# Performance work log

Measured on AMD Instinct MI355X. Metric: run time of the kernel, lower is better.

Reference implementation:

```python
import jax, jax.numpy as jnp
import numpy as np

N_G, E_G, E_H, E_I = 100000, 1000000, 1500000, 2000000
IN_FEATS = 64


def setup_inputs() -> dict:
    key = jax.random.key(0)
    ks = jax.random.split(key, 13)
    inp = {
        'z': jax.random.randint(ks[0], (N_G,), 0, 8),
        'src_g': jax.random.randint(ks[1], (E_G,), 0, N_G),
        'dst_g': jax.random.randint(ks[2], (E_G,), 0, N_G),
        'src_h': jax.random.randint(ks[3], (E_H,), 0, E_G),
        'dst_h': jax.random.randint(ks[4], (E_H,), 0, E_G),
        'src_i': jax.random.randint(ks[5], (E_I,), 0, E_H),
        'dst_i': jax.random.randint(ks[6], (E_I,), 0, E_H),
    }
    for n, k in zip(['e1', 'e2', 'e3', 'e4', 'e5', 'e6'], ks[7:13]):
        inp[n] = jax.random.normal(k, (2, IN_FEATS), dtype=jnp.float32)
    return inp


def reference(z, src_g, dst_g, src_h, dst_h, src_i, dst_i, e1, e2, e3, e4, e5, e6):
    # hop 1: g.apply_edges(send_z) -> per-edge endpoint labels, become h node data
    z_src = z[src_g]            # [E_G]
    z_dst = z[dst_g]            # [E_G]
    # hop 2: h.apply_edges(send_z2) -> become i node data
    z_src_src = z_src[src_h]    # [E_H]
    z_dst_dst = z_dst[dst_h]    # [E_H]
    # hop 3: i.apply_edges(comparison4) on edge endpoints of i
    za = z_src_src[src_i]       # [E_I]
    zb = z_src_src[dst_i]
    zc = z_dst_dst[src_i]
    zd = z_dst_dst[dst_i]
    zac = (za == zc).astype(jnp.int32)
    zab = (za == zb).astype(jnp.int32)
    zbc = (zc == zb).astype(jnp.int32)
    zad = (za == zd).astype(jnp.int32)
    zcd = (zc == zd).astype(jnp.int32)
    zbd = (zb == zd).astype(jnp.int32)
    # six 2-row embedding lookups summed -> [E_I, IN_FEATS]
    h = e1[zac] + e2[zab] + e3[zbc] + e4[zad] + e5[zcd] + e6[zbd]
    return h
```

## Files before the change

### kernel.cpp

```cpp
#include <hip/hip_runtime.h>


#define N_FEAT 64

__global__ void build_table_kernel(const float* __restrict__ e1,
                                   const float* __restrict__ e2,
                                   const float* __restrict__ e3,
                                   const float* __restrict__ e4,
                                   const float* __restrict__ e5,
                                   const float* __restrict__ e6,
                                   float* __restrict__ table) {
    int idx = blockIdx.x * blockDim.x + threadIdx.x;
    if (idx >= 64 * N_FEAT) return;
    int combo = idx >> 6;
    int f     = idx & (N_FEAT - 1);
    float v = e1[((combo >> 0) & 1) * N_FEAT + f];
    v      += e2[((combo >> 1) & 1) * N_FEAT + f];
    v      += e3[((combo >> 2) & 1) * N_FEAT + f];
    v      += e4[((combo >> 3) & 1) * N_FEAT + f];
    v      += e5[((combo >> 4) & 1) * N_FEAT + f];
    v      += e6[((combo >> 5) & 1) * N_FEAT + f];
    table[idx] = v;
}

__global__ void hop1_kernel(const int* __restrict__ z,
                            const int* __restrict__ src_g,
                            const int* __restrict__ dst_g,
                            uchar2* __restrict__ zg,
                            int n) {
    int e = blockIdx.x * blockDim.x + threadIdx.x;
    if (e >= n) return;
    uchar2 p;
    p.x = (unsigned char)z[src_g[e]];
    p.y = (unsigned char)z[dst_g[e]];
    zg[e] = p;
}

__global__ void hop2_kernel(const uchar2* __restrict__ zg,
                            const int* __restrict__ src_h,
                            const int* __restrict__ dst_h,
                            uchar2* __restrict__ zh,
                            int n) {
    int e = blockIdx.x * blockDim.x + threadIdx.x;
    if (e >= n) return;
    uchar2 p;
    p.x = zg[src_h[e]].x;
    p.y = zg[dst_h[e]].y;
    zh[e] = p;
}

__global__ void combo_kernel(const uchar2* __restrict__ zh,
                             const int* __restrict__ src_i,
                             const int* __restrict__ dst_i,
                             unsigned char* __restrict__ combo,
                             int n) {
    int e = blockIdx.x * blockDim.x + threadIdx.x;
    if (e >= n) return;
    uchar2 p = zh[src_i[e]];
    uchar2 q = zh[dst_i[e]];
    int za = p.x, zc = p.y, zb = q.x, zd = q.y;
    int cb = (int)(za == zc)
           | ((int)(za == zb) << 1)
           | ((int)(zc == zb) << 2)
           | ((int)(za == zd) << 3)
           | ((int)(zc == zd) << 4)
           | ((int)(zb == zd) << 5);
    combo[e] = (unsigned char)cb;
}

__global__ void write_kernel(const unsigned char* __restrict__ combo,
                             const float* __restrict__ table,
                             float* __restrict__ out,
                             int n) {
    long long t = (long long)blockIdx.x * blockDim.x + threadIdx.x;
    int e = (int)(t >> 4);
    int c = (int)(t & 15);
    if (e >= n) return;
    int cb = combo[e];
    const float4* row = (const float4*)(table + cb * N_FEAT);
    float4 v = row[c];
    float4* orow = (float4*)(out + (size_t)e * N_FEAT);
    orow[c] = v;
}

extern "C" void kernel_launch(void* const* d_in, const int* in_sizes, int n_in,
                              void* d_out, int out_size, void* d_ws, size_t ws_size,
                              hipStream_t stream) {
    const int* z     = (const int*)d_in[0];
    const int* src_g = (const int*)d_in[1];
    const int* dst_g = (const int*)d_in[2];
    const int* src_h = (const int*)d_in[3];
    const int* dst_h = (const int*)d_in[4];
    const int* src_i = (const int*)d_in[5];
    const int* dst_i = (const int*)d_in[6];
    const float* e1  = (const float*)d_in[7];
    const float* e2  = (const float*)d_in[8];
    const float* e3  = (const float*)d_in[9];
    const float* e4  = (const float*)d_in[10];
    const float* e5  = (const float*)d_in[11];
    const float* e6  = (const float*)d_in[12];

    const int E_G = in_sizes[1];
    const int E_H = in_sizes[3];
    const int E_I = in_sizes[5];

    char* ws = (char*)d_ws;
    float*  table = (float*)ws;
    size_t  off   = 64 * N_FEAT * sizeof(float);
    uchar2* zg    = (uchar2*)(ws + off);
    off += (size_t)E_G * sizeof(uchar2);
    off  = (off + 255) & ~(size_t)255;
    uchar2* zh    = (uchar2*)(ws + off);
    off += (size_t)E_H * sizeof(uchar2);
    off  = (off + 255) & ~(size_t)255;
    unsigned char* combo = (unsigned char*)(ws + off);

    float* out = (float*)d_out;

    build_table_kernel<<<16, 256, 0, stream>>>(e1, e2, e3, e4, e5, e6, table);

    hop1_kernel<<<(E_G + 255) / 256, 256, 0, stream>>>(z, src_g, dst_g, zg, E_G);

    hop2_kernel<<<(E_H + 255) / 256, 256, 0, stream>>>(zg, src_h, dst_h, zh, E_H);

    combo_kernel<<<(E_I + 255) / 256, 256, 0, stream>>>(zh, src_i, dst_i, combo, E_I);

    long long total = (long long)E_I * 16;
    int blocks = (int)((total + 255) / 256);
    write_kernel<<<blocks, 256, 0, stream>>>(combo, table, out, E_I);
}
```

Measured before the change: 151.8 us.

## Fuse all stages into one cooperative persistent kernel with grid syncs

Replaces the five separate launches (table build, hop1, hop2, combo, write) with a single cooperative kernel of 1024 blocks that runs each stage as a grid-stride loop, separated by grid-wide barriers. The gather stages now read four edge indices at once through int4 loads and write packed 16-bit label pairs in wider stores. This is meant to remove per-launch overhead and the tails between kernels. In exchange it adds three grid.sync barriers, and the write stage, which dominates, is limited to a fixed grid of persistent threads.

```diff
diff --git a/kernel.cpp b/kernel.cpp
--- a/kernel.cpp
+++ b/kernel.cpp
@@ -1,86 +1,121 @@
 #include <hip/hip_runtime.h>
+#include <hip/hip_cooperative_groups.h>
+
+namespace cg = cooperative_groups;
 
 
 #define N_FEAT 64
 
-__global__ void build_table_kernel(const float* __restrict__ e1,
-                                   const float* __restrict__ e2,
-                                   const float* __restrict__ e3,
-                                   const float* __restrict__ e4,
-                                   const float* __restrict__ e5,
-                                   const float* __restrict__ e6,
-                                   float* __restrict__ table) {
-    int idx = blockIdx.x * blockDim.x + threadIdx.x;
-    if (idx >= 64 * N_FEAT) return;
-    int combo = idx >> 6;
-    int f     = idx & (N_FEAT - 1);
-    float v = e1[((combo >> 0) & 1) * N_FEAT + f];
-    v      += e2[((combo >> 1) & 1) * N_FEAT + f];
-    v      += e3[((combo >> 2) & 1) * N_FEAT + f];
-    v      += e4[((combo >> 3) & 1) * N_FEAT + f];
-    v      += e5[((combo >> 4) & 1) * N_FEAT + f];
-    v      += e6[((combo >> 5) & 1) * N_FEAT + f];
-    table[idx] = v;
+__device__ __forceinline__ unsigned combo6(unsigned p, unsigned q) {
+    unsigned za = p & 0xffu, zc = p >> 8;
+    unsigned zb = q & 0xffu, zd = q >> 8;
+    return (unsigned)(za == zc)
+         | ((unsigned)(za == zb) << 1)
+         | ((unsigned)(zc == zb) << 2)
+         | ((unsigned)(za == zd) << 3)
+         | ((unsigned)(zc == zd) << 4)
+         | ((unsigned)(zb == zd) << 5);
 }
 
-__global__ void hop1_kernel(const int* __restrict__ z,
-                            const int* __restrict__ src_g,
-                            const int* __restrict__ dst_g,
-                            uchar2* __restrict__ zg,
-                            int n) {
-    int e = blockIdx.x * blockDim.x + threadIdx.x;
-    if (e >= n) return;
-    uchar2 p;
-    p.x = (unsigned char)z[src_g[e]];
-    p.y = (unsigned char)z[dst_g[e]];
-    zg[e] = p;
-}
+__global__ __launch_bounds__(256, 4)
+void fused_kernel(const int* __restrict__ z,
+                  const int* __restrict__ src_g,
+                  const int* __restrict__ dst_g,
+                  const int* __restrict__ src_h,
+                  const int* __restrict__ dst_h,
+                  const int* __restrict__ src_i,
+                  const int* __restrict__ dst_i,
+                  const float* __restrict__ e1,
+                  const float* __restrict__ e2,
+                  const float* __restrict__ e3,
+                  const float* __restrict__ e4,
+                  const float* __restrict__ e5,
+                  const float* __restrict__ e6,
+                  float* __restrict__ table,
+                  unsigned short* __restrict__ zg,
+                  unsigned short* __restrict__ zh,
+                  unsigned char* __restrict__ combo,
+                  float* __restrict__ out,
+                  int E_G, int E_H, int E_I) {
+    cg::grid_group grid = cg::this_grid();
+    const int tid = blockIdx.x * blockDim.x + threadIdx.x;
+    const int nth = gridDim.x * blockDim.x;
 
-__global__ void hop2_kernel(const uchar2* __restrict__ zg,
-                            const int* __restrict__ src_h,
-                            const int* __restrict__ dst_h,
-                            uchar2* __restrict__ zh,
-                            int n) {
-    int e = blockIdx.x * blockDim.x + threadIdx.x;
-    if (e >= n) return;
-    uchar2 p;
-    p.x = zg[src_h[e]].x;
-    p.y = zg[dst_h[e]].y;
-    zh[e] = p;
-}
+    for (int idx = tid; idx < 64 * N_FEAT; idx += nth) {
+        int cmb = idx >> 6;
+        int f   = idx & (N_FEAT - 1);
+        float v = e1[((cmb >> 0) & 1) * N_FEAT + f];
+        v      += e2[((cmb >> 1) & 1) * N_FEAT + f];
+        v      += e3[((cmb >> 2) & 1) * N_FEAT + f];
+        v      += e4[((cmb >> 3) & 1) * N_FEAT + f];
+        v      += e5[((cmb >> 4) & 1) * N_FEAT + f];
+        v      += e6[((cmb >> 5) & 1) * N_FEAT + f];
+        table[idx] = v;
+    }
 
-__global__ void combo_kernel(const uchar2* __restrict__ zh,
-                             const int* __restrict__ src_i,
-                             const int* __restrict__ dst_i,
-                             unsigned char* __restrict__ combo,
-                             int n) {
-    int e = blockIdx.x * blockDim.x + threadIdx.x;
-    if (e >= n) return;
-    uchar2 p = zh[src_i[e]];
-    uchar2 q = zh[dst_i[e]];
-    int za = p.x, zc = p.y, zb = q.x, zd = q.y;
-    int cb = (int)(za == zc)
-           | ((int)(za == zb) << 1)
-           | ((int)(zc == zb) << 2)
-           | ((int)(za == zd) << 3)
-           | ((int)(zc == zd) << 4)
-           | ((int)(zb == zd) << 5);
-    combo[e] = (unsigned char)cb;
-}
+    const int ng4 = E_G >> 2;
+    for (int i = tid; i < ng4; i += nth) {
+        int4 s = ((const int4*)src_g)[i];
+        int4 d = ((const int4*)dst_g)[i];
+        unsigned r0 = ((unsigned)z[s.x] & 0xffu)
+                    | (((unsigned)z[d.x] & 0xffu) << 8)
+                    | (((unsigned)z[s.y] & 0xffu) << 16)
+                    | (((unsigned)z[d.y] & 0xffu) << 24);
+        unsigned r1 = ((unsigned)z[s.z] & 0xffu)
+                    | (((unsigned)z[d.z] & 0xffu) << 8)
+                    | (((unsigned)z[s.w] & 0xffu) << 16)
+                    | (((unsigned)z[d.w] & 0xffu) << 24);
+        ((uint2*)zg)[i] = make_uint2(r0, r1);
+    }
+    for (int e = (ng4 << 2) + tid; e < E_G; e += nth) {
+        zg[e] = (unsigned short)(((unsigned)z[src_g[e]] & 0xffu)
+                               | (((unsigned)z[dst_g[e]] & 0xffu) << 8));
+    }
+    grid.sync();
 
-__global__ void write_kernel(const unsigned char* __restrict__ combo,
-                             const float* __restrict__ table,
-                             float* __restrict__ out,
-                             int n) {
-    long long t = (long long)blockIdx.x * blockDim.x + threadIdx.x;
-    int e = (int)(t >> 4);
-    int c = (int)(t & 15);
-    if (e >= n) return;
-    int cb = combo[e];
-    const float4* row = (const float4*)(table + cb * N_FEAT);
-    float4 v = row[c];
-    float4* orow = (float4*)(out + (size_t)e * N_FEAT);
-    orow[c] = v;
+    const int nh4 = E_H >> 2;
+    for (int i = tid; i < nh4; i += nth) {
+        int4 s = ((const int4*)src_h)[i];
+        int4 d = ((const int4*)dst_h)[i];
+        unsigned a0 = zg[s.x], b0 = zg[d.x];
+        unsigned a1 = zg[s.y], b1 = zg[d.y];
+        unsigned a2 = zg[s.z], b2 = zg[d.z];
+        unsigned a3 = zg[s.w], b3 = zg[d.w];
+        unsigned r0 = (a0 & 0xffu) | (b0 & 0xff00u)
+                    | ((a1 & 0xffu) << 16) | ((b1 & 0xff00u) << 16);
+        unsigned r1 = (a2 & 0xffu) | (b2 & 0xff00u)
+                    | ((a3 & 0xffu) << 16) | ((b3 & 0xff00u) << 16);
+        ((uint2*)zh)[i] = make_uint2(r0, r1);
+    }
+    for (int e = (nh4 << 2) + tid; e < E_H; e += nth) {
+        unsigned a = zg[src_h[e]], b = zg[dst_h[e]];
+        zh[e] = (unsigned short)((a & 0xffu) | (b & 0xff00u));
+    }
+    grid.sync();
+
+    const int ni4 = E_I >> 2;
+    for (int i = tid; i < ni4; i += nth) {
+        int4 s = ((const int4*)src_i)[i];
+        int4 d = ((const int4*)dst_i)[i];
+        unsigned c0 = combo6(zh[s.x], zh[d.x]);
+        unsigned c1 = combo6(zh[s.y], zh[d.y]);
+        unsigned c2 = combo6(zh[s.z], zh[d.z]);
+        unsigned c3 = combo6(zh[s.w], zh[d.w]);
+        ((unsigned*)combo)[i] = c0 | (c1 << 8) | (c2 << 16) | (c3 << 24);
+    }
+    for (int e = (ni4 << 2) + tid; e < E_I; e += nth) {
+        combo[e] = (unsigned char)combo6(zh[src_i[e]], zh[dst_i[e]]);
+    }
+    grid.sync();
+
+    const long long total = (long long)E_I * 16;
+    for (long long t = tid; t < total; t += nth) {
+        int e  = (int)(t >> 4);
+        int c  = (int)(t & 15);
+        int cb = combo[e];
+        float4 v = ((const float4*)(table + cb * N_FEAT))[c];
+        ((float4*)(out + (size_t)e * N_FEAT))[c] = v;
+    }
 }
 
 extern "C" void kernel_launch(void* const* d_in, const int* in_sizes, int n_in,
@@ -100,32 +135,31 @@
     const float* e5  = (const float*)d_in[11];
     const float* e6  = (const float*)d_in[12];
 
-    const int E_G = in_sizes[1];
-    const int E_H = in_sizes[3];
-    const int E_I = in_sizes[5];
+    int E_G = in_sizes[1];
+    int E_H = in_sizes[3];
+    int E_I = in_sizes[5];
 
     char* ws = (char*)d_ws;
-    float*  table = (float*)ws;
-    size_t  off   = 64 * N_FEAT * sizeof(float);
-    uchar2* zg    = (uchar2*)(ws + off);
-    off += (size_t)E_G * sizeof(uchar2);
+    float* table = (float*)ws;
+    size_t off   = 64 * N_FEAT * sizeof(float);
+    unsigned short* zg = (unsigned short*)(ws + off);
+    off += (size_t)E_G * sizeof(unsigned short);
     off  = (off + 255) & ~(size_t)255;
-    uchar2* zh    = (uchar2*)(ws + off);
-    off += (size_t)E_H * sizeof(uchar2);
+    unsigned short* zh = (unsigned short*)(ws + off);
+    off += (size_t)E_H * sizeof(unsigned short);
     off  = (off + 255) & ~(size_t)255;
     unsigned char* combo = (unsigned char*)(ws + off);
 
     float* out = (float*)d_out;
 
-    build_table_kernel<<<16, 256, 0, stream>>>(e1, e2, e3, e4, e5, e6, table);
+    void* args[] = {
+        (void*)&z, (void*)&src_g, (void*)&dst_g,
+        (void*)&src_h, (void*)&dst_h, (void*)&src_i, (void*)&dst_i,
+        (void*)&e1, (void*)&e2, (void*)&e3, (void*)&e4, (void*)&e5, (void*)&e6,
+        (void*)&table, (void*)&zg, (void*)&zh, (void*)&combo, (void*)&out,
+        (void*)&E_G, (void*)&E_H, (void*)&E_I
+    };
 
-    hop1_kernel<<<(E_G + 255) / 256, 256, 0, stream>>>(z, src_g, dst_g, zg, E_G);
-
-    hop2_kernel<<<(E_H + 255) / 256, 256, 0, stream>>>(zg, src_h, dst_h, zh, E_H);
-
-    combo_kernel<<<(E_I + 255) / 256, 256, 0, stream>>>(zh, src_i, dst_i, combo, E_I);
-
-    long long total = (long long)E_I * 16;
-    int blocks = (int)((total + 255) / 256);
-    write_kernel<<<blocks, 256, 0, stream>>>(combo, table, out, E_I);
+    hipLaunchCooperativeKernel((const void*)fused_kernel,
+                               dim3(1024), dim3(256), args, 0, stream);
 }
```

Result: slower. 541.4 us (+256.7%).
